# Performance work log

Hardware: AMD Instinct MI355X
Metric: run time of the kernel (lower is better)

The kernel has to match this reference:

```python
import jax, jax.numpy as jnp
import numpy as np

EPS = 1e-12  # F.normalize default eps


def _l2_normalize(v):
    # torch.nn.functional.normalize(v, dim=1): v / max(||v||_2, eps)
    n = jnp.sqrt(jnp.sum(v * v, axis=1, keepdims=True))
    return v / jnp.maximum(n, EPS)


def _max_cut_grad(x, src, dst, edge_weight, num_nodes):
    # MessagePassing(aggr='add'): message = x_j * w, scatter-add at dst
    msg = x[src] * edge_weight[:, None]          # [E, r]
    return jax.ops.segment_sum(msg, dst, num_segments=num_nodes)  # [N, r]


def setup_inputs() -> dict:
    key = jax.random.key(0)
    ks = jax.random.split(key, 8)
    N, E, r = 50000, 1600000, 32
    L_lift, L_proj = 8, 4
    x = jax.random.normal(ks[0], (N, r), dtype=jnp.float32)
    edge_index = jax.random.randint(ks[1], (2, E), 0, N, dtype=jnp.int64)
    edge_weight = jax.random.normal(ks[2], (E,), dtype=jnp.float32)
    s = 1.0 / np.sqrt(2 * r)
    lift_W = jax.random.uniform(ks[3], (L_lift, 2 * r, r), jnp.float32, -s, s)
    lift_b = jax.random.uniform(ks[4], (L_lift, r), jnp.float32, -s, s)
    proj_W = jax.random.uniform(ks[5], (L_proj, 2 * r, r), jnp.float32, -s, s)
    proj_b = jax.random.uniform(ks[6], (L_proj, r), jnp.float32, -s, s)
    return {"x": x, "edge_index": edge_index, "edge_weight": edge_weight,
            "lift_W": lift_W, "lift_b": lift_b, "proj_W": proj_W, "proj_b": proj_b}


def reference(x, edge_index, edge_weight, lift_W, lift_b, proj_W, proj_b):
    N = x.shape[0]
    src, dst = edge_index[0], edge_index[1]

    # Lift layers: grads -> normalize -> concat -> Linear -> normalize
    def lift_step(h, wb):
        W, b = wb
        g = _l2_normalize(_max_cut_grad(h, src, dst, edge_weight, N))
        out = jnp.concatenate([h, g], axis=1) @ W + b
        return _l2_normalize(out), None

    x, _ = jax.lax.scan(lift_step, x, (lift_W, lift_b))

    # Project layers: grads -> concat -> Linear -> tanh
    def proj_step(h, wb):
        W, b = wb
        g = _max_cut_grad(h, src, dst, edge_weight, N)
        out = jnp.concatenate([h, g], axis=1) @ W + b
        return jnp.tanh(out), None

    x, _ = jax.lax.scan(proj_step, x, (proj_W, proj_b))
    return x
```

## Files before the change

### kernel.cpp

```cpp
#include <hip/hip_runtime.h>
#include <hip/hip_fp16.h>
#include <math.h>


#define R 32
#define EPSN 1e-12f
#define BINW 256
#define CAP  9216
#define EPB  4096
#define NPB  16
#define GSTR 16

typedef unsigned short u16;
typedef unsigned int   u32;

__device__ __forceinline__ u16 f2h(float f) {
    return __half_as_ushort(__float2half_rn(f));
}

__launch_bounds__(1024)
__global__ void bin_scatter_kernel(const int* __restrict__ ei, const float* __restrict__ ew,
                                   int* __restrict__ gcur, int2* __restrict__ binned,
                                   int E, int nb) {
    __shared__ int lhist[BINW];
    __shared__ int lbase[BINW];
    __shared__ int lcur[BINW];
    const int tid = threadIdx.x;
    for (int i = tid; i < nb; i += 1024) { lhist[i] = 0; lcur[i] = 0; }
    __syncthreads();
    const int e0 = blockIdx.x * EPB;
    const int e1 = min(e0 + EPB, E);

    int dv[4], sv[4]; float wv[4];
    #pragma unroll
    for (int k = 0; k < 4; ++k) {
        const int e = e0 + tid + k * 1024;
        const bool ok = (e < e1);
        dv[k] = ok ? ei[E + e] : -1;
        sv[k] = ok ? ei[e] : 0;
        wv[k] = ok ? ew[e] : 0.f;
    }
    #pragma unroll
    for (int k = 0; k < 4; ++k)
        if (dv[k] >= 0) atomicAdd(&lhist[dv[k] >> 8], 1);
    __syncthreads();
    for (int i = tid; i < nb; i += 1024)
        lbase[i] = atomicAdd(&gcur[i * GSTR], lhist[i]);
    __syncthreads();
    #pragma unroll
    for (int k = 0; k < 4; ++k) {
        if (dv[k] < 0) continue;
        const int bin = dv[k] >> 8, dl = dv[k] & 255;
        const int slot = lbase[bin] + atomicAdd(&lcur[bin], 1);
        if (slot < CAP)
            binned[(size_t)bin * CAP + slot] = make_int2(sv[k] | (dl << 16), __float_as_int(wv[k]));
    }
}

__global__ void bin_scan_kernel(const int* __restrict__ gcur, int* __restrict__ binoff, int nb) {
    __shared__ int s[256];
    const int tid = threadIdx.x;
    const int v0 = (tid < nb) ? gcur[tid * GSTR] : 0;
    s[tid] = v0;
    __syncthreads();
    for (int off = 1; off < 256; off <<= 1) {
        int v = (tid >= off) ? s[tid - off] : 0;
        __syncthreads();
        s[tid] += v;
        __syncthreads();
    }
    if (tid < nb) binoff[tid] = s[tid] - v0;
}

__launch_bounds__(256)
__global__ void csr_build_kernel(const int2* __restrict__ binned, const int* __restrict__ gcur,
                                 const int* __restrict__ binoff,
                                 int* __restrict__ offsets, u32* __restrict__ csrp,
                                 int* __restrict__ bucket_cnt,
                                 int N, int E, int nb) {
    __shared__ int cnt[BINW];
    __shared__ int sc[BINW];
    __shared__ int excl[BINW];
    __shared__ int cur[BINW];
    __shared__ int bc8[8];
    const int b = blockIdx.x;
    const int tid = threadIdx.x;
    cnt[tid] = 0; cur[tid] = 0;
    if (tid < 8) bc8[tid] = 0;
    __syncthreads();
    const int2* src = binned + (size_t)b * CAP;
    const int n = gcur[b * GSTR];
    const int base = binoff[b];
    for (int i = tid; i < n; i += 256)
        atomicAdd(&cnt[((unsigned)src[i].x) >> 16], 1);
    __syncthreads();
    sc[tid] = cnt[tid];
    __syncthreads();
    for (int off = 1; off < 256; off <<= 1) {
        int v = (tid >= off) ? sc[tid - off] : 0;
        __syncthreads();
        sc[tid] += v;
        __syncthreads();
    }
    excl[tid] = sc[tid] - cnt[tid];
    const int node = b * BINW + tid;
    if (node < N) {
        offsets[node] = base + excl[tid];
        atomicAdd(&bc8[min(7, (cnt[tid] + 31) >> 5)], 1);
    }
    if (b == nb - 1 && tid == 0) offsets[N] = E;
    __syncthreads();
    if (tid < 8 && bc8[tid] > 0) atomicAdd(&bucket_cnt[tid * GSTR], bc8[tid]);
    for (int i = tid; i < n; i += 256) {
        const int2 p = src[i];
        const unsigned key = (unsigned)p.x;
        const int dl = key >> 16;
        const u32 s  = key & 0xffffu;
        const int slot = base + excl[dl] + atomicAdd(&cur[dl], 1);
        csrp[slot] = ((u32)f2h(__int_as_float(p.y)) << 16) | s;
    }
}

__global__ void bucket_scan_kernel(const int* __restrict__ bucket_cnt, int* __restrict__ bcur) {
    if (threadIdx.x == 0) {
        int run = 0;
        for (int i = 0; i < 8; ++i) { bcur[i * GSTR] = run; run += bucket_cnt[i * GSTR]; }
    }
}

__launch_bounds__(256)
__global__ void perm_fill_kernel(const int* __restrict__ offsets, int* __restrict__ bcur,
                                 int* __restrict__ perm, int N) {
    __shared__ int cnt8[8], base8[8], idx8[8];
    const int tid = threadIdx.x;
    const int node = blockIdx.x * 256 + tid;
    if (tid < 8) { cnt8[tid] = 0; idx8[tid] = 0; }
    __syncthreads();
    int wc = 0;
    if (node < N) {
        const int d = offsets[node + 1] - offsets[node];
        wc = min(7, (d + 31) >> 5);
        atomicAdd(&cnt8[wc], 1);
    }
    __syncthreads();
    if (tid < 8 && cnt8[tid] > 0) base8[tid] = atomicAdd(&bcur[tid * GSTR], cnt8[tid]);
    __syncthreads();
    if (node < N) {
        const int p = base8[wc] + atomicAdd(&idx8[wc], 1);
        perm[p] = node;
    }
}

__global__ void transpose_W_kernel(const float* __restrict__ liftW,
                                   const float* __restrict__ projW,
                                   float* __restrict__ WT) {
    const int l = blockIdx.x;
    const float* W = (l < 8) ? liftW + (size_t)l * 2048 : projW + (size_t)(l - 8) * 2048;
    float* T = WT + (size_t)l * 2048;
    for (int i = threadIdx.x; i < 2048; i += 256) {
        const int k = i >> 5, j = i & 31;
        T[j * 64 + k] = W[i];
    }
}

__global__ void cvt_x_kernel(const float* __restrict__ x, u16* __restrict__ xH, int total8) {
    const int t = blockIdx.x * 256 + threadIdx.x;
    if (t >= total8) return;
    const float4 v0 = reinterpret_cast<const float4*>(x)[t * 2];
    const float4 v1 = reinterpret_cast<const float4*>(x)[t * 2 + 1];
    u16 o[8] = { f2h(v0.x), f2h(v0.y), f2h(v0.z), f2h(v0.w),
                 f2h(v1.x), f2h(v1.y), f2h(v1.z), f2h(v1.w) };
    reinterpret_cast<uint4*>(xH)[t] = *reinterpret_cast<uint4*>(o);
}

template <bool LIFT, bool FINAL>
__launch_bounds__(512, 8)
__global__ void layer_kernel(const u16*  __restrict__ hH,
                             const int*  __restrict__ offsets,
                             const u32*  __restrict__ csrp,
                             const int*  __restrict__ perm,
                             const float* __restrict__ WT,
                             const float* __restrict__ bias,
                             u16*  __restrict__ outH,
                             float* __restrict__ outF,
                             int N) {
    __shared__ float WsT[32][68];
    __shared__ float hg[NPB][64];

    const int tid = threadIdx.x;
    {
        const float4 v = *reinterpret_cast<const float4*>(WT + tid * 4);
        *reinterpret_cast<float4*>(&WsT[tid >> 4][(tid & 15) * 4]) = v;
    }
    __syncthreads();

    const int grp   = tid >> 5;
    const int j     = tid & 31;
    const int sub   = j & 3;
    const int eslot = j >> 2;
    const unsigned fo = (unsigned)sub * 16u;
    const int node  = perm[blockIdx.x * NPB + grp];
    const char* hb  = (const char*)hH;

    hg[grp][j] = __half2float(((const __half*)hH)[(size_t)node * R + j]);

    const int beg = offsets[node];
    const int end = offsets[node + 1];
    float a0=0.f,a1=0.f,a2=0.f,a3=0.f,a4=0.f,a5=0.f,a6=0.f,a7=0.f;
    if (end > beg) {
        u32 q = csrp[min(beg + j, end - 1)];
        if (beg + j >= end) q &= 0xffffu;

        for (int base = beg; base < end; base += 32) {
            u32 qn = csrp[min(base + 32 + j, end - 1)];
            if (base + 32 + j >= end) qn &= 0xffffu;

            #pragma unroll
            for (int s = 0; s < 4; ++s) {
                const u32  qq = (u32)__shfl((int)q, s * 8 + eslot, 32);
                const float w = __half2float(__ushort_as_half((u16)(qq >> 16)));
                const uint4 hv = *reinterpret_cast<const uint4*>(hb + ((qq & 0xffffu) << 6) + fo);
                const float2 f01 = __half22float2(*reinterpret_cast<const __half2*>(&hv.x));
                const float2 f23 = __half22float2(*reinterpret_cast<const __half2*>(&hv.y));
                const float2 f45 = __half22float2(*reinterpret_cast<const __half2*>(&hv.z));
                const float2 f67 = __half22float2(*reinterpret_cast<const __half2*>(&hv.w));
                a0 = fmaf(f01.x, w, a0); a1 = fmaf(f01.y, w, a1);
                a2 = fmaf(f23.x, w, a2); a3 = fmaf(f23.y, w, a3);
                a4 = fmaf(f45.x, w, a4); a5 = fmaf(f45.y, w, a5);
                a6 = fmaf(f67.x, w, a6); a7 = fmaf(f67.y, w, a7);
            }
            q = qn;
        }
    }
    #pragma unroll
    for (int m = 4; m <= 16; m <<= 1) {
        a0 += __shfl_xor(a0, m, 32); a1 += __shfl_xor(a1, m, 32);
        a2 += __shfl_xor(a2, m, 32); a3 += __shfl_xor(a3, m, 32);
        a4 += __shfl_xor(a4, m, 32); a5 += __shfl_xor(a5, m, 32);
        a6 += __shfl_xor(a6, m, 32); a7 += __shfl_xor(a7, m, 32);
    }

    if (LIFT) {
        float ss = a0*a0 + a1*a1 + a2*a2 + a3*a3 + a4*a4 + a5*a5 + a6*a6 + a7*a7;
        ss += __shfl_xor(ss, 1, 32);
        ss += __shfl_xor(ss, 2, 32);
        const float sc = 1.f / fmaxf(sqrtf(ss), EPSN);
        a0 *= sc; a1 *= sc; a2 *= sc; a3 *= sc;
        a4 *= sc; a5 *= sc; a6 *= sc; a7 *= sc;
    }
    if (j < 4) {
        *reinterpret_cast<float4*>(&hg[grp][32 + j * 8])     = make_float4(a0, a1, a2, a3);
        *reinterpret_cast<float4*>(&hg[grp][32 + j * 8 + 4]) = make_float4(a4, a5, a6, a7);
    }

    float acc0 = bias[j], acc1 = 0.f;
    #pragma unroll
    for (int kb = 0; kb < 16; ++kb) {
        const float4 r  = *reinterpret_cast<const float4*>(&hg[grp][kb * 4]);
        const float4 wv = *reinterpret_cast<const float4*>(&WsT[j][kb * 4]);
        float& acc = (kb & 1) ? acc1 : acc0;
        acc = fmaf(r.x, wv.x, acc);
        acc = fmaf(r.y, wv.y, acc);
        acc = fmaf(r.z, wv.z, acc);
        acc = fmaf(r.w, wv.w, acc);
    }
    float acc = acc0 + acc1;

    if (LIFT) {
        float s = acc * acc;
        #pragma unroll
        for (int o = 16; o >= 1; o >>= 1) s += __shfl_xor(s, o, 32);
        acc = acc / fmaxf(sqrtf(s), EPSN);
    } else {
        acc = tanhf(acc);
    }

    if (FINAL)
        outF[(size_t)node * R + j] = acc;
    else
        outH[(size_t)node * R + j] = f2h(acc);
}

extern "C" void kernel_launch(void* const* d_in, const int* in_sizes, int n_in,
                              void* d_out, int out_size, void* d_ws, size_t ws_size,
                              hipStream_t stream) {
    const float* x      = (const float*)d_in[0];
    const int*   ei     = (const int*)d_in[1];
    const float* ew     = (const float*)d_in[2];
    const float* lift_W = (const float*)d_in[3];
    const float* lift_b = (const float*)d_in[4];
    const float* proj_W = (const float*)d_in[5];
    const float* proj_b = (const float*)d_in[6];

    const int N = in_sizes[0] / R;
    const int E = in_sizes[2];
    const int nb = (N + BINW - 1) / BINW;

    int*   offsets = (int*)d_ws;
    int*   gcur    = offsets + N + 1;
    int*   binoff  = gcur + 256 * GSTR;
    int*   bcnt    = binoff + 256;
    int*   bcur    = bcnt + 8 * GSTR;
    int*   perm    = bcur + 8 * GSTR;
    float* WT      = (float*)(perm + N);
    uintptr_t p    = (uintptr_t)(WT + 12 * 2048);
    p = (p + 15) & ~(uintptr_t)15;
    int2*  binned  = (int2*)p;
    u32*   csrp    = (u32*)(binned + (size_t)nb * CAP);
    u16*   xH      = (u16*)binned;
    u16*   hHa     = xH  + (size_t)N * R;
    u16*   hHb     = hHa + (size_t)N * R;

    const size_t ctr_ints = 256 * GSTR + 256 + 8 * GSTR + 8 * GSTR;
    hipMemsetAsync(gcur, 0, ctr_ints * sizeof(int), stream);
    transpose_W_kernel<<<12, 256, 0, stream>>>(lift_W, proj_W, WT);
    bin_scatter_kernel<<<(E + EPB - 1) / EPB, 1024, 0, stream>>>(ei, ew, gcur, binned, E, nb);
    bin_scan_kernel<<<1, 256, 0, stream>>>(gcur, binoff, nb);
    csr_build_kernel<<<nb, 256, 0, stream>>>(binned, gcur, binoff, offsets, csrp, bcnt, N, E, nb);
    bucket_scan_kernel<<<1, 64, 0, stream>>>(bcnt, bcur);
    perm_fill_kernel<<<nb, 256, 0, stream>>>(offsets, bcur, perm, N);
    const int total8 = N * R / 8;
    cvt_x_kernel<<<(total8 + 255) / 256, 256, 0, stream>>>(x, xH, total8);

    const u16* curH = xH;
    float* fout = (float*)d_out;
    const int node_blocks = N / NPB;

    for (int l = 0; l < 12; ++l) {
        const float* Wc = WT + (size_t)l * 2048;
        const float* b  = (l < 8) ? (lift_b + (size_t)l * R) : (proj_b + (size_t)(l - 8) * R);
        u16* dstH = (l & 1) ? hHb : hHa;
        if (l < 8)
            layer_kernel<true , false><<<node_blocks, 512, 0, stream>>>(curH, offsets, csrp, perm, Wc, b, dstH, nullptr, N);
        else if (l < 11)
            layer_kernel<false, false><<<node_blocks, 512, 0, stream>>>(curH, offsets, csrp, perm, Wc, b, dstH, nullptr, N);
        else
            layer_kernel<false, true ><<<node_blocks, 512, 0, stream>>>(curH, offsets, csrp, perm, Wc, b, nullptr, fout, N);
        curH = dstH;
    }
}
```

Measured before the change: 406.4 us.

## Sort nodes into finer degree buckets and skip empty gather sub-steps

Degree buckets for the node permutation now have a width of 8 edges instead of 32, with 16 buckets, so the nodes grouped into one block have closer degrees. The gather loop now counts its steps in groups of 8 edges and stops partway through a 32-edge chunk. This avoids wasted shuffles and loads on padded slots whose weight is zero. The transposed weight tile in shared memory also drops its padding for an XOR swizzle, which saves LDS while avoiding bank conflicts. The risk is that the variable inner trip count adds branching and may unroll less well.

```diff
diff --git a/kernel.cpp b/kernel.cpp
--- a/kernel.cpp
+++ b/kernel.cpp
@@ -10,6 +10,7 @@
 #define EPB  4096
 #define NPB  16
 #define GSTR 16
+#define NBK  16
 
 typedef unsigned short u16;
 typedef unsigned int   u32;
@@ -82,11 +83,11 @@
     __shared__ int sc[BINW];
     __shared__ int excl[BINW];
     __shared__ int cur[BINW];
-    __shared__ int bc8[8];
+    __shared__ int bcl[NBK];
     const int b = blockIdx.x;
     const int tid = threadIdx.x;
     cnt[tid] = 0; cur[tid] = 0;
-    if (tid < 8) bc8[tid] = 0;
+    if (tid < NBK) bcl[tid] = 0;
     __syncthreads();
     const int2* src = binned + (size_t)b * CAP;
     const int n = gcur[b * GSTR];
@@ -106,11 +107,11 @@
     const int node = b * BINW + tid;
     if (node < N) {
         offsets[node] = base + excl[tid];
-        atomicAdd(&bc8[min(7, (cnt[tid] + 31) >> 5)], 1);
+        atomicAdd(&bcl[min(NBK - 1, (cnt[tid] + 7) >> 3)], 1);
     }
     if (b == nb - 1 && tid == 0) offsets[N] = E;
     __syncthreads();
-    if (tid < 8 && bc8[tid] > 0) atomicAdd(&bucket_cnt[tid * GSTR], bc8[tid]);
+    if (tid < NBK && bcl[tid] > 0) atomicAdd(&bucket_cnt[tid * GSTR], bcl[tid]);
     for (int i = tid; i < n; i += 256) {
         const int2 p = src[i];
         const unsigned key = (unsigned)p.x;
@@ -124,29 +125,29 @@
 __global__ void bucket_scan_kernel(const int* __restrict__ bucket_cnt, int* __restrict__ bcur) {
     if (threadIdx.x == 0) {
         int run = 0;
-        for (int i = 0; i < 8; ++i) { bcur[i * GSTR] = run; run += bucket_cnt[i * GSTR]; }
+        for (int i = 0; i < NBK; ++i) { bcur[i * GSTR] = run; run += bucket_cnt[i * GSTR]; }
     }
 }
 
 __launch_bounds__(256)
 __global__ void perm_fill_kernel(const int* __restrict__ offsets, int* __restrict__ bcur,
                                  int* __restrict__ perm, int N) {
-    __shared__ int cnt8[8], base8[8], idx8[8];
+    __shared__ int cnt16[NBK], base16[NBK], idx16[NBK];
     const int tid = threadIdx.x;
     const int node = blockIdx.x * 256 + tid;
-    if (tid < 8) { cnt8[tid] = 0; idx8[tid] = 0; }
+    if (tid < NBK) { cnt16[tid] = 0; idx16[tid] = 0; }
     __syncthreads();
     int wc = 0;
     if (node < N) {
         const int d = offsets[node + 1] - offsets[node];
-        wc = min(7, (d + 31) >> 5);
-        atomicAdd(&cnt8[wc], 1);
-    }
-    __syncthreads();
-    if (tid < 8 && cnt8[tid] > 0) base8[tid] = atomicAdd(&bcur[tid * GSTR], cnt8[tid]);
+        wc = min(NBK - 1, (d + 7) >> 3);
+        atomicAdd(&cnt16[wc], 1);
+    }
+    __syncthreads();
+    if (tid < NBK && cnt16[tid] > 0) base16[tid] = atomicAdd(&bcur[tid * GSTR], cnt16[tid]);
     __syncthreads();
     if (node < N) {
-        const int p = base8[wc] + atomicAdd(&idx8[wc], 1);
+        const int p = base16[wc] + atomicAdd(&idx16[wc], 1);
         perm[p] = node;
     }
 }
@@ -184,13 +185,14 @@
                              u16*  __restrict__ outH,
                              float* __restrict__ outF,
                              int N) {
-    __shared__ float WsT[32][68];
+    __shared__ float WsT[32 * 64];
     __shared__ float hg[NPB][64];
 
     const int tid = threadIdx.x;
     {
         const float4 v = *reinterpret_cast<const float4*>(WT + tid * 4);
-        *reinterpret_cast<float4*>(&WsT[tid >> 4][(tid & 15) * 4]) = v;
+        const int j4 = tid >> 4, k4 = tid & 15;
+        reinterpret_cast<float4*>(WsT)[j4 * 16 + (k4 ^ (j4 & 7))] = v;
     }
     __syncthreads();
 
@@ -206,17 +208,20 @@
 
     const int beg = offsets[node];
     const int end = offsets[node + 1];
+    const int nsteps = (end - beg + 7) >> 3;
     float a0=0.f,a1=0.f,a2=0.f,a3=0.f,a4=0.f,a5=0.f,a6=0.f,a7=0.f;
-    if (end > beg) {
+    if (nsteps > 0) {
         u32 q = csrp[min(beg + j, end - 1)];
         if (beg + j >= end) q &= 0xffffu;
 
-        for (int base = beg; base < end; base += 32) {
+        int base = beg, sdone = 0;
+        while (sdone < nsteps) {
             u32 qn = csrp[min(base + 32 + j, end - 1)];
             if (base + 32 + j >= end) qn &= 0xffffu;
 
-            #pragma unroll
-            for (int s = 0; s < 4; ++s) {
+            const int sh = min(4, nsteps - sdone);
+            #pragma unroll 4
+            for (int s = 0; s < sh; ++s) {
                 const u32  qq = (u32)__shfl((int)q, s * 8 + eslot, 32);
                 const float w = __half2float(__ushort_as_half((u16)(qq >> 16)));
                 const uint4 hv = *reinterpret_cast<const uint4*>(hb + ((qq & 0xffffu) << 6) + fo);
@@ -230,6 +235,7 @@
                 a6 = fmaf(f67.x, w, a6); a7 = fmaf(f67.y, w, a7);
             }
             q = qn;
+            base += 32; sdone += 4;
         }
     }
     #pragma unroll
@@ -257,7 +263,7 @@
     #pragma unroll
     for (int kb = 0; kb < 16; ++kb) {
         const float4 r  = *reinterpret_cast<const float4*>(&hg[grp][kb * 4]);
-        const float4 wv = *reinterpret_cast<const float4*>(&WsT[j][kb * 4]);
+        const float4 wv = reinterpret_cast<const float4*>(WsT)[j * 16 + (kb ^ (j & 7))];
         float& acc = (kb & 1) ? acc1 : acc0;
         acc = fmaf(r.x, wv.x, acc);
         acc = fmaf(r.y, wv.y, acc);
@@ -300,8 +306,8 @@
     int*   gcur    = offsets + N + 1;
     int*   binoff  = gcur + 256 * GSTR;
     int*   bcnt    = binoff + 256;
-    int*   bcur    = bcnt + 8 * GSTR;
-    int*   perm    = bcur + 8 * GSTR;
+    int*   bcur    = bcnt + NBK * GSTR;
+    int*   perm    = bcur + NBK * GSTR;
     float* WT      = (float*)(perm + N);
     uintptr_t p    = (uintptr_t)(WT + 12 * 2048);
     p = (p + 15) & ~(uintptr_t)15;
@@ -311,7 +317,7 @@
     u16*   hHa     = xH  + (size_t)N * R;
     u16*   hHb     = hHa + (size_t)N * R;
 
-    const size_t ctr_ints = 256 * GSTR + 256 + 8 * GSTR + 8 * GSTR;
+    const size_t ctr_ints = 256 * GSTR + 256 + 2 * NBK * GSTR;
     hipMemsetAsync(gcur, 0, ctr_ints * sizeof(int), stream);
     transpose_W_kernel<<<12, 256, 0, stream>>>(lift_W, proj_W, WT);
     bin_scatter_kernel<<<(E + EPB - 1) / EPB, 1024, 0, stream>>>(ei, ew, gcur, binned, E, nb);
```

Measured after the change: 411.2 us. Within noise of the previous version (+1.2%).
